# Kernel optimization log

Hardware: AMD Instinct MI355X
Metric: run time of the kernel (lower is better)

Reference implementation:

```python
import jax, jax.numpy as jnp
import numpy as np

B, S, D, H, KVH = 1, 2048, 4096, 32, 8
HD = D // H  # head_dim = 128
ROPE_THETA = 500000.0
NEG_INF = -1e9


def setup_inputs() -> dict:
    key = jax.random.key(0)
    ks = jax.random.split(key, 5)
    x = jax.random.normal(ks[0], (B, S, D), jnp.float32)
    wq = jax.random.normal(ks[1], (D, H * HD), jnp.float32) * 0.02
    wk = jax.random.normal(ks[2], (D, KVH * HD), jnp.float32) * 0.02
    wv = jax.random.normal(ks[3], (D, KVH * HD), jnp.float32) * 0.02
    wo = jax.random.normal(ks[4], (H * HD, D), jnp.float32) * 0.02
    inv = 1.0 / (ROPE_THETA ** (np.arange(0, HD, 2, dtype=np.float32) / HD))
    ang = np.arange(S, dtype=np.float32)[:, None] * inv[None, :]  # [S, HD/2]
    return dict(x=x, wq=wq, wk=wk, wv=wv, wo=wo,
                freqs_cos=jnp.asarray(np.cos(ang)), freqs_sin=jnp.asarray(np.sin(ang)))


def _rope(t, cos, sin):
    # t: [B, S, h, HD]; complex rotation on even/odd interleaved pairs
    tr = t.reshape(*t.shape[:-1], HD // 2, 2)
    t0, t1 = tr[..., 0], tr[..., 1]
    c = cos[None, :, None, :]
    s = sin[None, :, None, :]
    o0 = t0 * c - t1 * s
    o1 = t0 * s + t1 * c
    return jnp.stack([o0, o1], axis=-1).reshape(t.shape)


def reference(x, wq, wk, wv, wo, freqs_cos, freqs_sin):
    # QKV projections (prefill path: seqlen>1, start_pos=0 -> causal flash attn)
    xq = (x @ wq).reshape(B, S, H, HD)
    xk = (x @ wk).reshape(B, S, KVH, HD)
    xv = (x @ wv).reshape(B, S, KVH, HD)
    xq = _rope(xq, freqs_cos, freqs_sin)
    xk = _rope(xk, freqs_cos, freqs_sin)
    # GQA: repeat kv heads to match query heads
    n_rep = H // KVH
    xk = jnp.repeat(xk, n_rep, axis=2)  # [B,S,H,HD]
    xv = jnp.repeat(xv, n_rep, axis=2)
    scale = 1.0 / jnp.sqrt(jnp.asarray(HD, xq.dtype))
    scores = jnp.einsum('bqhd,bkhd->bhqk', xq, xk) * scale
    causal = jnp.tril(jnp.ones((S, S), bool))
    scores = jnp.where(causal[None, None], scores, NEG_INF)
    probs = jax.nn.softmax(scores, axis=-1)
    out = jnp.einsum('bhqk,bkhd->bqhd', probs, xv)  # [B,S,H,HD]
    return out.reshape(B, S, H * HD) @ wo
```

## Files before the change

### kernel.cpp

```cpp
#include <hip/hip_runtime.h>
#include <type_traits>

typedef __attribute__((ext_vector_type(8))) short short8;
typedef __attribute__((ext_vector_type(4))) float float4v;

__device__ inline float bf2f(short s) {
    unsigned u = ((unsigned)(unsigned short)s) << 16;
    float f; __builtin_memcpy(&f, &u, 4); return f;
}
__device__ inline short f2bf(float f) {
    unsigned u; __builtin_memcpy(&u, &f, 4);
    unsigned lsb = (u >> 16) & 1;
    u += 0x7fffu + lsb;
    return (short)(u >> 16);
}

__device__ inline void glds16(const void* g, void* l) {
    __builtin_amdgcn_global_load_lds(
        (const __attribute__((address_space(1))) unsigned int*)g,
        (__attribute__((address_space(3))) unsigned int*)l, 16, 0, 0);
}

__global__ __launch_bounds__(256) void conv_f32_bf16(const float* __restrict__ in,
                                                     short* __restrict__ out, int n8) {
    int idx = blockIdx.x * 256 + threadIdx.x;
    if (idx >= n8) return;
    const float* src = in + (size_t)idx * 8;
    float4v a = *(const float4v*)src;
    float4v b = *(const float4v*)(src + 4);
    short8 o;
#pragma unroll
    for (int j = 0; j < 4; j++) { o[j] = f2bf(a[j]); o[4 + j] = f2bf(b[j]); }
    *(short8*)(out + (size_t)idx * 8) = o;
}

__global__ __launch_bounds__(256) void transpose_conv(const float* __restrict__ in,
                                                      short* __restrict__ out,
                                                      int K, int ldn, int noff) {
    __shared__ float t[64 * 65];
    const int n0 = blockIdx.x * 64, k0 = blockIdx.y * 64;
    const int tid = threadIdx.x;
#pragma unroll
    for (int i = 0; i < 4; i++) {
        int slot = tid + 256 * i;
        int row = slot >> 4, c4 = slot & 15;
        float4v v = *(const float4v*)(in + (size_t)(k0 + row) * ldn + noff + n0 + c4 * 4);
#pragma unroll
        for (int j = 0; j < 4; j++) t[row * 65 + c4 * 4 + j] = v[j];
    }
    __syncthreads();
#pragma unroll
    for (int i = 0; i < 2; i++) {
        int slot = tid + 256 * i;
        int row = slot >> 3, c8 = slot & 7;
        short8 v;
#pragma unroll
        for (int j = 0; j < 8; j++) v[j] = f2bf(t[(c8 * 8 + j) * 65 + row]);
        *(short8*)(out + (size_t)(n0 + row) * K + k0 + c8 * 8) = v;
    }
}

__global__ __launch_bounds__(256) void transpose_k(const short* __restrict__ in,
                                                   short* __restrict__ out,
                                                   int K, int N, int ldin) {
    __attribute__((aligned(16))) __shared__ short t[64 * 72];
    const int n0 = blockIdx.x * 64, k0 = blockIdx.y * 64;
    const int tid = threadIdx.x;
#pragma unroll
    for (int i = 0; i < 2; i++) {
        int slot = tid + 256 * i;
        int row = slot >> 3, c8 = slot & 7;
        *(short8*)&t[row * 72 + c8 * 8] =
            *(const short8*)(in + (size_t)(k0 + row) * ldin + n0 + c8 * 8);
    }
    __syncthreads();
#pragma unroll
    for (int i = 0; i < 2; i++) {
        int slot = tid + 256 * i;
        int row = slot >> 3, c8 = slot & 7;
        short8 v;
#pragma unroll
        for (int j = 0; j < 8; j++) v[j] = t[(c8 * 8 + j) * 72 + row];
        *(short8*)(out + (size_t)(n0 + row) * K + k0 + c8 * 8) = v;
    }
}

template <typename CT>
__global__ __launch_bounds__(512) void gemm_bt_p(const short* __restrict__ A,
                                                 const short* __restrict__ Bt,
                                                 CT* __restrict__ C) {
    __attribute__((aligned(16))) __shared__ short lds[2][(128 + 256) * 64];
    const int tid = threadIdx.x;
    const int lane = tid & 63, wave = tid >> 6;
    const int quad = lane >> 4, l16 = lane & 15;
    const int wm = wave >> 2, wn = wave & 3;
    const int b = blockIdx.x;
    const int sw = (b & 7) * 32 + (b >> 3);
    const int n0 = (sw & 15) * 256;
    const int m0 = (sw >> 4) * 128;
    const int lr = lane >> 3, lc = lane & 7;
    const int swc = lc ^ lr;
    const int K = 4096;

    float4v acc[4][4];
#pragma unroll
    for (int i = 0; i < 4; i++)
#pragma unroll
        for (int j = 0; j < 4; j++) acc[i][j] = (float4v){0.f, 0.f, 0.f, 0.f};

    auto stage = [&](int t, int buf) {
        const int k0 = t * 64;
        short* Ab = &lds[buf][0];
        short* Bb = &lds[buf][128 * 64];
#pragma unroll
        for (int p = 0; p < 2; p++) {
            int row = p * 64 + wave * 8;
            glds16(A + (size_t)(m0 + row + lr) * K + k0 + swc * 8, Ab + row * 64);
        }
#pragma unroll
        for (int p = 0; p < 4; p++) {
            int row = p * 64 + wave * 8;
            glds16(Bt + (size_t)(n0 + row + lr) * K + k0 + swc * 8, Bb + row * 64);
        }
    };

    stage(0, 0);
    stage(1, 1);

    for (int t = 0; t < 64; t++) {
        if (t + 1 < 64) asm volatile("s_waitcnt vmcnt(6)" ::: "memory");
        else            asm volatile("s_waitcnt vmcnt(0)" ::: "memory");
        __builtin_amdgcn_sched_barrier(0);
        __builtin_amdgcn_s_barrier();
        asm volatile("" ::: "memory");
        const short* As = &lds[t & 1][0];
        const short* Bs = &lds[t & 1][128 * 64];
        short8 af[4][2], bf[4][2];
#pragma unroll
        for (int mf = 0; mf < 4; mf++)
#pragma unroll
            for (int kc = 0; kc < 2; kc++)
                af[mf][kc] = *(const short8*)&As[(wm * 64 + mf * 16 + l16) * 64 +
                                                 (((kc * 4 + quad) ^ (l16 & 7)) * 8)];
#pragma unroll
        for (int nf = 0; nf < 4; nf++)
#pragma unroll
            for (int kc = 0; kc < 2; kc++)
                bf[nf][kc] = *(const short8*)&Bs[(wn * 64 + nf * 16 + l16) * 64 +
                                                 (((kc * 4 + quad) ^ (l16 & 7)) * 8)];
        __builtin_amdgcn_s_setprio(1);
#pragma unroll
        for (int mf = 0; mf < 4; mf++)
#pragma unroll
            for (int nf = 0; nf < 4; nf++)
#pragma unroll
                for (int kc = 0; kc < 2; kc++)
                    acc[mf][nf] = __builtin_amdgcn_mfma_f32_16x16x32_bf16(
                        af[mf][kc], bf[nf][kc], acc[mf][nf], 0, 0, 0);
        __builtin_amdgcn_s_setprio(0);
        asm volatile("" ::: "memory");
        __builtin_amdgcn_s_barrier();
        asm volatile("" ::: "memory");
        if (t + 2 < 64) stage(t + 2, t & 1);
    }

#pragma unroll
    for (int mf = 0; mf < 4; mf++)
#pragma unroll
        for (int nf = 0; nf < 4; nf++) {
            int col = n0 + wn * 64 + nf * 16 + l16;
#pragma unroll
            for (int r = 0; r < 4; r++) {
                int row = m0 + wm * 64 + mf * 16 + quad * 4 + r;
                if constexpr (std::is_same<CT, float>::value)
                    C[(size_t)row * 4096 + col] = acc[mf][nf][r];
                else
                    C[(size_t)row * 4096 + col] = f2bf(acc[mf][nf][r]);
            }
        }
}

template <typename AT, typename CT>
__global__ __launch_bounds__(256) void gemm_bt_g(const AT* __restrict__ A,
                                                 const short* __restrict__ Bt,
                                                 CT* __restrict__ C,
                                                 int K, int ldc, int coff) {
    __attribute__((aligned(16))) __shared__ short As[128 * 64];
    __attribute__((aligned(16))) __shared__ short Bs[128 * 64];
    const int tid = threadIdx.x;
    const int lane = tid & 63, wave = tid >> 6;
    const int quad = lane >> 4, l16 = lane & 15;
    const int wr = wave >> 1, wc = wave & 1;
    const int m0 = blockIdx.y * 128, n0 = blockIdx.x * 128;
    const int lrow = lane >> 3, lc8 = lane & 7;

    float4v acc[4][4];
#pragma unroll
    for (int i = 0; i < 4; i++)
#pragma unroll
        for (int j = 0; j < 4; j++) acc[i][j] = (float4v){0.f, 0.f, 0.f, 0.f};

    for (int k0 = 0; k0 < K; k0 += 64) {
#pragma unroll
        for (int r = 0; r < 4; r++) {
            int slab = r * 4 + wave;
            glds16(Bt + (size_t)(n0 + slab * 8 + lrow) * K + k0 + lc8 * 8, &Bs[slab * 512]);
        }
        if constexpr (std::is_same<AT, short>::value) {
#pragma unroll
            for (int r = 0; r < 4; r++) {
                int slab = r * 4 + wave;
                glds16(A + (size_t)(m0 + slab * 8 + lrow) * K + k0 + lc8 * 8, &As[slab * 512]);
            }
        } else {
#pragma unroll
            for (int i = 0; i < 4; i++) {
                int slot = tid + 256 * i;
                int row = slot >> 3, c8 = slot & 7;
                const float* src = A + (size_t)(m0 + row) * K + k0 + c8 * 8;
                float4v a = *(const float4v*)src;
                float4v b = *(const float4v*)(src + 4);
                short8 o;
#pragma unroll
                for (int j = 0; j < 4; j++) { o[j] = f2bf(a[j]); o[4 + j] = f2bf(b[j]); }
                *(short8*)&As[row * 64 + c8 * 8] = o;
            }
        }
        __syncthreads();
#pragma unroll
        for (int kc = 0; kc < 2; kc++) {
            short8 afr[4], bfr[4];
#pragma unroll
            for (int rt = 0; rt < 4; rt++)
                afr[rt] = *(const short8*)&As[(wr * 64 + rt * 16 + l16) * 64 + kc * 32 + quad * 8];
#pragma unroll
            for (int ct = 0; ct < 4; ct++)
                bfr[ct] = *(const short8*)&Bs[(wc * 64 + ct * 16 + l16) * 64 + kc * 32 + quad * 8];
#pragma unroll
            for (int rt = 0; rt < 4; rt++)
#pragma unroll
                for (int ct = 0; ct < 4; ct++)
                    acc[rt][ct] = __builtin_amdgcn_mfma_f32_16x16x32_bf16(
                        afr[rt], bfr[ct], acc[rt][ct], 0, 0, 0);
        }
        __syncthreads();
    }
#pragma unroll
    for (int rt = 0; rt < 4; rt++)
#pragma unroll
        for (int ct = 0; ct < 4; ct++) {
            int col = coff + n0 + wc * 64 + ct * 16 + l16;
#pragma unroll
            for (int r = 0; r < 4; r++) {
                int row = m0 + wr * 64 + rt * 16 + quad * 4 + r;
                if constexpr (std::is_same<CT, float>::value)
                    C[(size_t)row * ldc + col] = acc[rt][ct][r];
                else
                    C[(size_t)row * ldc + col] = f2bf(acc[rt][ct][r]);
            }
        }
}

__global__ void rope_kernel(short* __restrict__ T, const float* __restrict__ cosb,
                            const float* __restrict__ sinb, int nheads, int ld) {
    int idx = blockIdx.x * 256 + threadIdx.x;
    int total = 2048 * nheads * 16;
    if (idx >= total) return;
    int chunk = idx & 15;
    int t2 = idx >> 4;
    int hh = t2 % nheads;
    int s = t2 / nheads;
    short* p = T + (size_t)s * ld + hh * 128 + chunk * 8;
    short8 v = *(short8*)p;
    short8 o;
#pragma unroll
    for (int t = 0; t < 4; t++) {
        int i = chunk * 4 + t;
        float c = cosb[s * 64 + i];
        float sn = sinb[s * 64 + i];
        float a = bf2f(v[2 * t]), b = bf2f(v[2 * t + 1]);
        o[2 * t] = f2bf(a * c - b * sn);
        o[2 * t + 1] = f2bf(a * sn + b * c);
    }
    *(short8*)p = o;
}

__global__ __launch_bounds__(256) void attn_kernel(const short* __restrict__ Q,
                                                   const short* __restrict__ K,
                                                   const short* __restrict__ Vt,
                                                   short* __restrict__ O, int ldk) {
    __attribute__((aligned(16))) __shared__ short Ks[64 * 128];
    __attribute__((aligned(16))) __shared__ short Vs[128 * 64];
    __attribute__((aligned(16))) __shared__ short Ps[4][16 * 72];
    const int tid = threadIdx.x;
    const int lane = tid & 63, wave = tid >> 6;
    const int quad = lane >> 4, l16 = lane & 15;
    const int h = blockIdx.y, kvh = h >> 2;
    const float scale = 0.08838834764831845f;

    for (int pass = 0; pass < 2; pass++) {
        const int qtile = pass ? (31 - (int)blockIdx.x) : (int)blockIdx.x;
        const int qbase = qtile * 64;
        const int q0 = qbase + wave * 16;
        const int nt = qtile + 1;

        short8 qf[4];
        const short* qrow = Q + (size_t)(q0 + l16) * 4096 + h * 128;
#pragma unroll
        for (int ks = 0; ks < 4; ks++) qf[ks] = *(const short8*)(qrow + ks * 32 + quad * 8);

        float4v o_acc[8];
#pragma unroll
        for (int i = 0; i < 8; i++) o_acc[i] = (float4v){0.f, 0.f, 0.f, 0.f};
        float m_i[4], l_i[4];
#pragma unroll
        for (int r = 0; r < 4; r++) { m_i[r] = -1e9f; l_i[r] = 0.f; }

        short8 kreg[4], vreg[4];
#pragma unroll
        for (int i = 0; i < 4; i++) {
            int slot = tid + 256 * i;
            int row = slot >> 4, c8 = slot & 15;
            kreg[i] = *(const short8*)(K + (size_t)row * ldk + kvh * 128 + c8 * 8);
        }
#pragma unroll
        for (int i = 0; i < 4; i++) {
            int slot = tid + 256 * i;
            int row = slot >> 3, c8 = slot & 7;
            vreg[i] = *(const short8*)(Vt + (size_t)(kvh * 128 + row) * 2048 + c8 * 8);
        }

        for (int t = 0; t < nt; t++) {
            const int kv0 = t * 64;
            __syncthreads();
#pragma unroll
            for (int i = 0; i < 4; i++) {
                int slot = tid + 256 * i;
                int row = slot >> 4, c8 = slot & 15;
                *(short8*)&Ks[row * 128 + ((c8 ^ (row & 15)) * 8)] = kreg[i];
            }
#pragma unroll
            for (int i = 0; i < 4; i++) {
                int slot = tid + 256 * i;
                int row = slot >> 3, c8 = slot & 7;
                *(short8*)&Vs[row * 64 + ((c8 ^ (row & 7)) * 8)] = vreg[i];
            }
            __syncthreads();
            if (t + 1 < nt) {
                const int kv1 = kv0 + 64;
#pragma unroll
                for (int i = 0; i < 4; i++) {
                    int slot = tid + 256 * i;
                    int row = slot >> 4, c8 = slot & 15;
                    kreg[i] = *(const short8*)(K + (size_t)(kv1 + row) * ldk + kvh * 128 + c8 * 8);
                }
#pragma unroll
                for (int i = 0; i < 4; i++) {
                    int slot = tid + 256 * i;
                    int row = slot >> 3, c8 = slot & 7;
                    vreg[i] = *(const short8*)(Vt + (size_t)(kvh * 128 + row) * 2048 + kv1 + c8 * 8);
                }
            }

            float4v s_acc[4];
#pragma unroll
            for (int i = 0; i < 4; i++) s_acc[i] = (float4v){0.f, 0.f, 0.f, 0.f};
            __builtin_amdgcn_s_setprio(1);
#pragma unroll
            for (int nsub = 0; nsub < 4; nsub++) {
                const int row = nsub * 16 + l16;
#pragma unroll
                for (int ks = 0; ks < 4; ks++) {
                    short8 kf = *(const short8*)&Ks[row * 128 + (((ks * 4 + quad) ^ l16) * 8)];
                    s_acc[nsub] = __builtin_amdgcn_mfma_f32_16x16x32_bf16(
                        qf[ks], kf, s_acc[nsub], 0, 0, 0);
                }
            }
            __builtin_amdgcn_s_setprio(0);

            const bool diag = (t == nt - 1);
            float p[4][4];
#pragma unroll
            for (int nsub = 0; nsub < 4; nsub++)
#pragma unroll
                for (int r = 0; r < 4; r++) {
                    float v = s_acc[nsub][r] * scale;
                    if (diag) {
                        int rowq = q0 + quad * 4 + r;
                        int col = kv0 + nsub * 16 + l16;
                        v = (col <= rowq) ? v : -1e9f;
                    }
                    p[nsub][r] = v;
                }
            float tm[4];
#pragma unroll
            for (int r = 0; r < 4; r++)
                tm[r] = fmaxf(fmaxf(p[0][r], p[1][r]), fmaxf(p[2][r], p[3][r]));
#pragma unroll
            for (int off = 1; off < 16; off <<= 1)
#pragma unroll
                for (int r = 0; r < 4; r++)
                    tm[r] = fmaxf(tm[r], __shfl_xor(tm[r], off, 64));
            float alpha[4], rs[4];
#pragma unroll
            for (int r = 0; r < 4; r++) {
                float mn = fmaxf(m_i[r], tm[r]);
                alpha[r] = __expf(m_i[r] - mn);
                m_i[r] = mn;
                rs[r] = 0.f;
            }
#pragma unroll
            for (int nsub = 0; nsub < 4; nsub++)
#pragma unroll
                for (int r = 0; r < 4; r++) {
                    float e = __expf(p[nsub][r] - m_i[r]);
                    rs[r] += e;
                    Ps[wave][(quad * 4 + r) * 72 + nsub * 16 + l16] = f2bf(e);
                }
#pragma unroll
            for (int off = 1; off < 16; off <<= 1)
#pragma unroll
                for (int r = 0; r < 4; r++) rs[r] += __shfl_xor(rs[r], off, 64);
#pragma unroll
            for (int r = 0; r < 4; r++) l_i[r] = l_i[r] * alpha[r] + rs[r];
#pragma unroll
            for (int dt = 0; dt < 8; dt++)
#pragma unroll
                for (int r = 0; r < 4; r++) o_acc[dt][r] *= alpha[r];

            short8 pf0 = *(const short8*)&Ps[wave][l16 * 72 + quad * 8];
            short8 pf1 = *(const short8*)&Ps[wave][l16 * 72 + 32 + quad * 8];
            __builtin_amdgcn_s_setprio(1);
#pragma unroll
            for (int dt = 0; dt < 8; dt++) {
                const int row = dt * 16 + l16;
                short8 vf0 = *(const short8*)&Vs[row * 64 + ((quad ^ (l16 & 7)) * 8)];
                short8 vf1 = *(const short8*)&Vs[row * 64 + (((4 + quad) ^ (l16 & 7)) * 8)];
                o_acc[dt] = __builtin_amdgcn_mfma_f32_16x16x32_bf16(pf0, vf0, o_acc[dt], 0, 0, 0);
                o_acc[dt] = __builtin_amdgcn_mfma_f32_16x16x32_bf16(pf1, vf1, o_acc[dt], 0, 0, 0);
            }
            __builtin_amdgcn_s_setprio(0);
        }

#pragma unroll
        for (int dt = 0; dt < 8; dt++)
#pragma unroll
            for (int r = 0; r < 4; r++) {
                int rowq = q0 + quad * 4 + r;
                O[(size_t)rowq * 4096 + h * 128 + dt * 16 + l16] = f2bf(o_acc[dt][r] / l_i[r]);
            }
    }
}

extern "C" void kernel_launch(void* const* d_in, const int* in_sizes, int n_in,
                              void* d_out, int out_size, void* d_ws, size_t ws_size,
                              hipStream_t stream) {
    (void)in_sizes; (void)n_in; (void)out_size;
    const float* x  = (const float*)d_in[0];
    const float* wq = (const float*)d_in[1];
    const float* wk = (const float*)d_in[2];
    const float* wv = (const float*)d_in[3];
    const float* wo = (const float*)d_in[4];
    const float* fc = (const float*)d_in[5];
    const float* fs = (const float*)d_in[6];
    float* out = (float*)d_out;
    char* ws = (char*)d_ws;
    const size_t MB = 1ull << 20;

    if (ws_size >= 76 * MB) {
        short* xb  = (short*)(ws);
        short* Qb  = (short*)(ws + 16 * MB);
        short* KVb = (short*)(ws + 32 * MB);
        short* Vt  = (short*)(ws + 40 * MB);
        short* WT  = (short*)(ws + 44 * MB);
        conv_f32_bf16<<<4096, 256, 0, stream>>>(x, xb, 2048 * 4096 / 8);
        transpose_conv<<<dim3(64, 64), 256, 0, stream>>>(wq, WT, 4096, 4096, 0);
        gemm_bt_p<short><<<256, 512, 0, stream>>>(xb, WT, Qb);
        transpose_conv<<<dim3(16, 64), 256, 0, stream>>>(wk, WT, 4096, 1024, 0);
        transpose_conv<<<dim3(16, 64), 256, 0, stream>>>(wv, WT + (size_t)1024 * 4096, 4096, 1024, 0);
        gemm_bt_g<short, short><<<dim3(16, 16), 256, 0, stream>>>(xb, WT, KVb, 4096, 2048, 0);
        rope_kernel<<<4096, 256, 0, stream>>>(Qb, fc, fs, 32, 4096);
        rope_kernel<<<1024, 256, 0, stream>>>(KVb, fc, fs, 8, 2048);
        transpose_k<<<dim3(16, 32), 256, 0, stream>>>(KVb + 1024, Vt, 2048, 1024, 2048);
        attn_kernel<<<dim3(16, 32), 256, 0, stream>>>(Qb, KVb, Vt, Qb, 2048);
        transpose_conv<<<dim3(64, 64), 256, 0, stream>>>(wo, WT, 4096, 4096, 0);
        gemm_bt_p<float><<<256, 512, 0, stream>>>(Qb, WT, out);
    } else if (ws_size >= 60 * MB) {
        short* xb  = (short*)(ws);
        short* Qb  = (short*)(ws + 16 * MB);
        short* KVb = (short*)(ws + 32 * MB);
        short* Vt  = (short*)(ws + 40 * MB);
        short* WT  = (short*)(ws + 44 * MB);
        conv_f32_bf16<<<4096, 256, 0, stream>>>(x, xb, 2048 * 4096 / 8);
        for (int s = 0; s < 2; s++) {
            transpose_conv<<<dim3(32, 64), 256, 0, stream>>>(wq, WT, 4096, 4096, s * 2048);
            gemm_bt_g<short, short><<<dim3(16, 16), 256, 0, stream>>>(xb, WT, Qb, 4096, 4096, s * 2048);
        }
        transpose_conv<<<dim3(16, 64), 256, 0, stream>>>(wk, WT, 4096, 1024, 0);
        transpose_conv<<<dim3(16, 64), 256, 0, stream>>>(wv, WT + (size_t)1024 * 4096, 4096, 1024, 0);
        gemm_bt_g<short, short><<<dim3(16, 16), 256, 0, stream>>>(xb, WT, KVb, 4096, 2048, 0);
        rope_kernel<<<4096, 256, 0, stream>>>(Qb, fc, fs, 32, 4096);
        rope_kernel<<<1024, 256, 0, stream>>>(KVb, fc, fs, 8, 2048);
        transpose_k<<<dim3(16, 32), 256, 0, stream>>>(KVb + 1024, Vt, 2048, 1024, 2048);
        attn_kernel<<<dim3(16, 32), 256, 0, stream>>>(Qb, KVb, Vt, Qb, 2048);
        for (int s = 0; s < 2; s++) {
            transpose_conv<<<dim3(32, 64), 256, 0, stream>>>(wo, WT, 4096, 4096, s * 2048);
            gemm_bt_g<short, float><<<dim3(16, 16), 256, 0, stream>>>(Qb, WT, out, 4096, 4096, s * 2048);
        }
    } else {
        short* WT = (short*)(ws);
        short* Qb = (short*)(ws + 8 * MB);
        short* Kb = (short*)(ws + 24 * MB);
        short* Vb = (short*)(ws + 28 * MB);
        short* Vt = (short*)(ws + 32 * MB);
        for (int s = 0; s < 4; s++) {
            transpose_conv<<<dim3(16, 64), 256, 0, stream>>>(wq, WT, 4096, 4096, s * 1024);
            gemm_bt_g<float, short><<<dim3(8, 16), 256, 0, stream>>>(x, WT, Qb, 4096, 4096, s * 1024);
        }
        transpose_conv<<<dim3(16, 64), 256, 0, stream>>>(wk, WT, 4096, 1024, 0);
        gemm_bt_g<float, short><<<dim3(8, 16), 256, 0, stream>>>(x, WT, Kb, 4096, 1024, 0);
        transpose_conv<<<dim3(16, 64), 256, 0, stream>>>(wv, WT, 4096, 1024, 0);
        gemm_bt_g<float, short><<<dim3(8, 16), 256, 0, stream>>>(x, WT, Vb, 4096, 1024, 0);
        rope_kernel<<<4096, 256, 0, stream>>>(Qb, fc, fs, 32, 4096);
        rope_kernel<<<1024, 256, 0, stream>>>(Kb, fc, fs, 8, 1024);
        transpose_k<<<dim3(16, 32), 256, 0, stream>>>(Vb, Vt, 2048, 1024, 1024);
        attn_kernel<<<dim3(16, 32), 256, 0, stream>>>(Qb, Kb, Vt, Qb, 1024);
        for (int s = 0; s < 4; s++) {
            transpose_conv<<<dim3(16, 64), 256, 0, stream>>>(wo, WT, 4096, 4096, s * 1024);
            gemm_bt_g<short, float><<<dim3(8, 16), 256, 0, stream>>>(Qb, WT, out, 4096, 4096, s * 1024);
        }
    }
}
```

Baseline: 542.2 us.

## Template pipelined GEMM for KV projection and double-buffer attention K/V tiles

Generalizes the 512-thread pipelined GEMM with template tile parameters and uses a 64x256-tile variant for the fused K/V projection instead of the simpler generic GEMM. In attention, K/V tiles are double-buffered in LDS so the next tile is written after compute, removing one barrier per iteration. Softmax switches to exp2 with a pre-scaled log2e factor, and the rescale of the accumulator is skipped when no row maximum changed across the wave. Double-buffering doubles attention LDS use, which may reduce occupancy.

```diff
diff --git a/kernel.cpp b/kernel.cpp
--- a/kernel.cpp
+++ b/kernel.cpp
@@ -85,35 +85,38 @@
     }
 }
 
-template <typename CT>
+template <int MF, int NB, typename CT>
 __global__ __launch_bounds__(512) void gemm_bt_p(const short* __restrict__ A,
                                                  const short* __restrict__ Bt,
                                                  CT* __restrict__ C) {
-    __attribute__((aligned(16))) __shared__ short lds[2][(128 + 256) * 64];
+    constexpr int BM = MF * 32;
+    constexpr int LDC = NB * 256;
+    constexpr int APASS = BM / 64;
+    __attribute__((aligned(16))) __shared__ short lds[2][(BM + 256) * 64];
     const int tid = threadIdx.x;
     const int lane = tid & 63, wave = tid >> 6;
     const int quad = lane >> 4, l16 = lane & 15;
     const int wm = wave >> 2, wn = wave & 3;
     const int b = blockIdx.x;
     const int sw = (b & 7) * 32 + (b >> 3);
-    const int n0 = (sw & 15) * 256;
-    const int m0 = (sw >> 4) * 128;
+    const int n0 = (sw % NB) * 256;
+    const int m0 = (sw / NB) * BM;
     const int lr = lane >> 3, lc = lane & 7;
     const int swc = lc ^ lr;
     const int K = 4096;
 
-    float4v acc[4][4];
-#pragma unroll
-    for (int i = 0; i < 4; i++)
+    float4v acc[MF][4];
+#pragma unroll
+    for (int i = 0; i < MF; i++)
 #pragma unroll
         for (int j = 0; j < 4; j++) acc[i][j] = (float4v){0.f, 0.f, 0.f, 0.f};
 
     auto stage = [&](int t, int buf) {
         const int k0 = t * 64;
         short* Ab = &lds[buf][0];
-        short* Bb = &lds[buf][128 * 64];
-#pragma unroll
-        for (int p = 0; p < 2; p++) {
+        short* Bb = &lds[buf][BM * 64];
+#pragma unroll
+        for (int p = 0; p < APASS; p++) {
             int row = p * 64 + wave * 8;
             glds16(A + (size_t)(m0 + row + lr) * K + k0 + swc * 8, Ab + row * 64);
         }
@@ -128,19 +131,23 @@
     stage(1, 1);
 
     for (int t = 0; t < 64; t++) {
-        if (t + 1 < 64) asm volatile("s_waitcnt vmcnt(6)" ::: "memory");
-        else            asm volatile("s_waitcnt vmcnt(0)" ::: "memory");
+        if (t + 1 < 64) {
+            if constexpr (APASS == 2) asm volatile("s_waitcnt vmcnt(6)" ::: "memory");
+            else                      asm volatile("s_waitcnt vmcnt(5)" ::: "memory");
+        } else {
+            asm volatile("s_waitcnt vmcnt(0)" ::: "memory");
+        }
         __builtin_amdgcn_sched_barrier(0);
         __builtin_amdgcn_s_barrier();
         asm volatile("" ::: "memory");
         const short* As = &lds[t & 1][0];
-        const short* Bs = &lds[t & 1][128 * 64];
-        short8 af[4][2], bf[4][2];
-#pragma unroll
-        for (int mf = 0; mf < 4; mf++)
+        const short* Bs = &lds[t & 1][BM * 64];
+        short8 af[MF][2], bf[4][2];
+#pragma unroll
+        for (int mf = 0; mf < MF; mf++)
 #pragma unroll
             for (int kc = 0; kc < 2; kc++)
-                af[mf][kc] = *(const short8*)&As[(wm * 64 + mf * 16 + l16) * 64 +
+                af[mf][kc] = *(const short8*)&As[(wm * MF * 16 + mf * 16 + l16) * 64 +
                                                  (((kc * 4 + quad) ^ (l16 & 7)) * 8)];
 #pragma unroll
         for (int nf = 0; nf < 4; nf++)
@@ -150,7 +157,7 @@
                                                  (((kc * 4 + quad) ^ (l16 & 7)) * 8)];
         __builtin_amdgcn_s_setprio(1);
 #pragma unroll
-        for (int mf = 0; mf < 4; mf++)
+        for (int mf = 0; mf < MF; mf++)
 #pragma unroll
             for (int nf = 0; nf < 4; nf++)
 #pragma unroll
@@ -165,17 +172,17 @@
     }
 
 #pragma unroll
-    for (int mf = 0; mf < 4; mf++)
+    for (int mf = 0; mf < MF; mf++)
 #pragma unroll
         for (int nf = 0; nf < 4; nf++) {
             int col = n0 + wn * 64 + nf * 16 + l16;
 #pragma unroll
             for (int r = 0; r < 4; r++) {
-                int row = m0 + wm * 64 + mf * 16 + quad * 4 + r;
+                int row = m0 + wm * MF * 16 + mf * 16 + quad * 4 + r;
                 if constexpr (std::is_same<CT, float>::value)
-                    C[(size_t)row * 4096 + col] = acc[mf][nf][r];
+                    C[(size_t)row * LDC + col] = acc[mf][nf][r];
                 else
-                    C[(size_t)row * 4096 + col] = f2bf(acc[mf][nf][r]);
+                    C[(size_t)row * LDC + col] = f2bf(acc[mf][nf][r]);
             }
         }
 }
@@ -289,14 +296,14 @@
                                                    const short* __restrict__ K,
                                                    const short* __restrict__ Vt,
                                                    short* __restrict__ O, int ldk) {
-    __attribute__((aligned(16))) __shared__ short Ks[64 * 128];
-    __attribute__((aligned(16))) __shared__ short Vs[128 * 64];
+    __attribute__((aligned(16))) __shared__ short Ks[2][64 * 128];
+    __attribute__((aligned(16))) __shared__ short Vs[2][128 * 64];
     __attribute__((aligned(16))) __shared__ short Ps[4][16 * 72];
     const int tid = threadIdx.x;
     const int lane = tid & 63, wave = tid >> 6;
     const int quad = lane >> 4, l16 = lane & 15;
     const int h = blockIdx.y, kvh = h >> 2;
-    const float scale = 0.08838834764831845f;
+    const float scale2 = 0.08838834764831845f * 1.4426950408889634f;
 
     for (int pass = 0; pass < 2; pass++) {
         const int qtile = pass ? (31 - (int)blockIdx.x) : (int)blockIdx.x;
@@ -329,24 +336,26 @@
             int row = slot >> 3, c8 = slot & 7;
             vreg[i] = *(const short8*)(Vt + (size_t)(kvh * 128 + row) * 2048 + c8 * 8);
         }
+        __syncthreads();
+#pragma unroll
+        for (int i = 0; i < 4; i++) {
+            int slot = tid + 256 * i;
+            int row = slot >> 4, c8 = slot & 15;
+            *(short8*)&Ks[0][row * 128 + ((c8 ^ (row & 15)) * 8)] = kreg[i];
+        }
+#pragma unroll
+        for (int i = 0; i < 4; i++) {
+            int slot = tid + 256 * i;
+            int row = slot >> 3, c8 = slot & 7;
+            *(short8*)&Vs[0][row * 64 + ((c8 ^ (row & 7)) * 8)] = vreg[i];
+        }
 
         for (int t = 0; t < nt; t++) {
             const int kv0 = t * 64;
+            const int cur = t & 1;
             __syncthreads();
-#pragma unroll
-            for (int i = 0; i < 4; i++) {
-                int slot = tid + 256 * i;
-                int row = slot >> 4, c8 = slot & 15;
-                *(short8*)&Ks[row * 128 + ((c8 ^ (row & 15)) * 8)] = kreg[i];
-            }
-#pragma unroll
-            for (int i = 0; i < 4; i++) {
-                int slot = tid + 256 * i;
-                int row = slot >> 3, c8 = slot & 7;
-                *(short8*)&Vs[row * 64 + ((c8 ^ (row & 7)) * 8)] = vreg[i];
-            }
-            __syncthreads();
-            if (t + 1 < nt) {
+            const bool pf = (t + 1 < nt);
+            if (pf) {
                 const int kv1 = kv0 + 64;
 #pragma unroll
                 for (int i = 0; i < 4; i++) {
@@ -371,7 +380,7 @@
                 const int row = nsub * 16 + l16;
 #pragma unroll
                 for (int ks = 0; ks < 4; ks++) {
-                    short8 kf = *(const short8*)&Ks[row * 128 + (((ks * 4 + quad) ^ l16) * 8)];
+                    short8 kf = *(const short8*)&Ks[cur][row * 128 + (((ks * 4 + quad) ^ l16) * 8)];
                     s_acc[nsub] = __builtin_amdgcn_mfma_f32_16x16x32_bf16(
                         qf[ks], kf, s_acc[nsub], 0, 0, 0);
                 }
@@ -384,7 +393,7 @@
             for (int nsub = 0; nsub < 4; nsub++)
 #pragma unroll
                 for (int r = 0; r < 4; r++) {
-                    float v = s_acc[nsub][r] * scale;
+                    float v = s_acc[nsub][r] * scale2;
                     if (diag) {
                         int rowq = q0 + quad * 4 + r;
                         int col = kv0 + nsub * 16 + l16;
@@ -401,19 +410,27 @@
 #pragma unroll
                 for (int r = 0; r < 4; r++)
                     tm[r] = fmaxf(tm[r], __shfl_xor(tm[r], off, 64));
-            float alpha[4], rs[4];
-#pragma unroll
-            for (int r = 0; r < 4; r++) {
-                float mn = fmaxf(m_i[r], tm[r]);
-                alpha[r] = __expf(m_i[r] - mn);
-                m_i[r] = mn;
-                rs[r] = 0.f;
-            }
+            int ok = 1;
+#pragma unroll
+            for (int r = 0; r < 4; r++) ok &= (tm[r] <= m_i[r]);
+            const bool need = !__all(ok);
+            float alpha[4];
+            if (need) {
+#pragma unroll
+                for (int r = 0; r < 4; r++) {
+                    float mn = fmaxf(m_i[r], tm[r]);
+                    alpha[r] = __builtin_amdgcn_exp2f(m_i[r] - mn);
+                    m_i[r] = mn;
+                }
+            }
+            float rs[4];
+#pragma unroll
+            for (int r = 0; r < 4; r++) rs[r] = 0.f;
 #pragma unroll
             for (int nsub = 0; nsub < 4; nsub++)
 #pragma unroll
                 for (int r = 0; r < 4; r++) {
-                    float e = __expf(p[nsub][r] - m_i[r]);
+                    float e = __builtin_amdgcn_exp2f(p[nsub][r] - m_i[r]);
                     rs[r] += e;
                     Ps[wave][(quad * 4 + r) * 72 + nsub * 16 + l16] = f2bf(e);
                 }
@@ -421,12 +438,17 @@
             for (int off = 1; off < 16; off <<= 1)
 #pragma unroll
                 for (int r = 0; r < 4; r++) rs[r] += __shfl_xor(rs[r], off, 64);
-#pragma unroll
-            for (int r = 0; r < 4; r++) l_i[r] = l_i[r] * alpha[r] + rs[r];
-#pragma unroll
-            for (int dt = 0; dt < 8; dt++)
-#pragma unroll
-                for (int r = 0; r < 4; r++) o_acc[dt][r] *= alpha[r];
+            if (need) {
+#pragma unroll
+                for (int r = 0; r < 4; r++) l_i[r] = l_i[r] * alpha[r] + rs[r];
+#pragma unroll
+                for (int dt = 0; dt < 8; dt++)
+#pragma unroll
+                    for (int r = 0; r < 4; r++) o_acc[dt][r] *= alpha[r];
+            } else {
+#pragma unroll
+                for (int r = 0; r < 4; r++) l_i[r] += rs[r];
+            }
 
             short8 pf0 = *(const short8*)&Ps[wave][l16 * 72 + quad * 8];
             short8 pf1 = *(const short8*)&Ps[wave][l16 * 72 + 32 + quad * 8];
@@ -434,12 +456,27 @@
 #pragma unroll
             for (int dt = 0; dt < 8; dt++) {
                 const int row = dt * 16 + l16;
-                short8 vf0 = *(const short8*)&Vs[row * 64 + ((quad ^ (l16 & 7)) * 8)];
-                short8 vf1 = *(const short8*)&Vs[row * 64 + (((4 + quad) ^ (l16 & 7)) * 8)];
+                short8 vf0 = *(const short8*)&Vs[cur][row * 64 + ((quad ^ (l16 & 7)) * 8)];
+                short8 vf1 = *(const short8*)&Vs[cur][row * 64 + (((4 + quad) ^ (l16 & 7)) * 8)];
                 o_acc[dt] = __builtin_amdgcn_mfma_f32_16x16x32_bf16(pf0, vf0, o_acc[dt], 0, 0, 0);
                 o_acc[dt] = __builtin_amdgcn_mfma_f32_16x16x32_bf16(pf1, vf1, o_acc[dt], 0, 0, 0);
             }
             __builtin_amdgcn_s_setprio(0);
+
+            if (pf) {
+#pragma unroll
+                for (int i = 0; i < 4; i++) {
+                    int slot = tid + 256 * i;
+                    int row = slot >> 4, c8 = slot & 15;
+                    *(short8*)&Ks[cur ^ 1][row * 128 + ((c8 ^ (row & 15)) * 8)] = kreg[i];
+                }
+#pragma unroll
+                for (int i = 0; i < 4; i++) {
+                    int slot = tid + 256 * i;
+                    int row = slot >> 3, c8 = slot & 7;
+                    *(short8*)&Vs[cur ^ 1][row * 64 + ((c8 ^ (row & 7)) * 8)] = vreg[i];
+                }
+            }
         }
 
 #pragma unroll
@@ -475,16 +512,16 @@
         short* WT  = (short*)(ws + 44 * MB);
         conv_f32_bf16<<<4096, 256, 0, stream>>>(x, xb, 2048 * 4096 / 8);
         transpose_conv<<<dim3(64, 64), 256, 0, stream>>>(wq, WT, 4096, 4096, 0);
-        gemm_bt_p<short><<<256, 512, 0, stream>>>(xb, WT, Qb);
+        gemm_bt_p<4, 16, short><<<256, 512, 0, stream>>>(xb, WT, Qb);
         transpose_conv<<<dim3(16, 64), 256, 0, stream>>>(wk, WT, 4096, 1024, 0);
         transpose_conv<<<dim3(16, 64), 256, 0, stream>>>(wv, WT + (size_t)1024 * 4096, 4096, 1024, 0);
-        gemm_bt_g<short, short><<<dim3(16, 16), 256, 0, stream>>>(xb, WT, KVb, 4096, 2048, 0);
+        gemm_bt_p<2, 8, short><<<256, 512, 0, stream>>>(xb, WT, KVb);
         rope_kernel<<<4096, 256, 0, stream>>>(Qb, fc, fs, 32, 4096);
         rope_kernel<<<1024, 256, 0, stream>>>(KVb, fc, fs, 8, 2048);
         transpose_k<<<dim3(16, 32), 256, 0, stream>>>(KVb + 1024, Vt, 2048, 1024, 2048);
         attn_kernel<<<dim3(16, 32), 256, 0, stream>>>(Qb, KVb, Vt, Qb, 2048);
         transpose_conv<<<dim3(64, 64), 256, 0, stream>>>(wo, WT, 4096, 4096, 0);
-        gemm_bt_p<float><<<256, 512, 0, stream>>>(Qb, WT, out);
+        gemm_bt_p<4, 16, float><<<256, 512, 0, stream>>>(Qb, WT, out);
     } else if (ws_size >= 60 * MB) {
         short* xb  = (short*)(ws);
         short* Qb  = (short*)(ws + 16 * MB);
```

New measurement: 567.4 us. +4.6%, slower.
